# Optimization experiments

Hardware: AMD Instinct MI355X
Metric: run time of the kernel (lower is better)

## Reference

```python
import jax, jax.numpy as jnp
import numpy as np

B, S, D, H = 2, 2048, 2048, 16
HD = D // H  # 128


def setup_inputs() -> dict:
    key = jax.random.key(0)
    ks = jax.random.split(key, 6)
    sc = 0.02
    return {
        "x": jax.random.normal(ks[0], (B, S, D), jnp.float32),
        "attention_mask": jnp.ones((B, S), jnp.int32),
        "w_qkv": jax.random.normal(ks[1], (D, 3 * D), jnp.float32) * sc,
        "b_qkv": jnp.zeros((3 * D,), jnp.float32),
        "w_o": jax.random.normal(ks[2], (D, D), jnp.float32) * sc,
        "b_o": jnp.zeros((D,), jnp.float32),
        "ln1_w": jnp.ones((D,), jnp.float32),
        "w1": jax.random.normal(ks[3], (D, 8 * D), jnp.float32) * sc,
        "b1": jnp.zeros((8 * D,), jnp.float32),
        "w2": jax.random.normal(ks[4], (4 * D, D), jnp.float32) * sc,
        "b2": jnp.zeros((D,), jnp.float32),
        "ln2_w": jnp.ones((D,), jnp.float32),
    }


def rmsnorm(x, w, eps=1e-6):
    rms = jnp.sqrt(jnp.mean(x * x, axis=-1, keepdims=True) + eps)
    return w * (x / rms)


def rope_tables(seq_len, dim, base=10000.0):
    inv_freq = 1.0 / (base ** (jnp.arange(0, dim, 2, dtype=jnp.float32) / dim))
    t = jnp.arange(seq_len, dtype=jnp.float32)
    freqs = t[:, None] * inv_freq[None, :]          # [S, dim/2]
    emb = jnp.concatenate([freqs, freqs], axis=-1)  # [S, dim]
    return jnp.cos(emb), jnp.sin(emb)


def apply_rope(x, cos, sin):
    # Faithful to source: rotate pairs, then out = rot*cos + roll(rot,1)*sin
    xr = x.reshape(*x.shape[:-1], -1, 2)
    x1, x2 = xr[..., 0], xr[..., 1]
    rot = jnp.stack([-x2, x1], axis=-1).reshape(x.shape)
    return rot * cos + jnp.roll(rot, shift=1, axis=-1) * sin


def transformer_layer(x, attention_mask, w_qkv, b_qkv, w_o, b_o, ln1_w, w1, b1, w2, b2, ln2_w):
    residual = x
    qkv = x @ w_qkv + b_qkv                         # [B,S,3D]
    q, k, v = jnp.split(qkv, 3, axis=-1)
    split = lambda t: t.reshape(B, S, H, HD).transpose(0, 2, 1, 3)  # [B,H,S,HD]
    q, k, v = split(q), split(k), split(v)

    cos, sin = rope_tables(S, HD)                   # [S,HD], broadcasts over B,H
    q = apply_rope(q, cos, sin)
    k = apply_rope(k, cos, sin)

    scores = jnp.einsum("bhqd,bhkd->bhqk", q, k) / jnp.sqrt(jnp.float32(HD))
    mask = (attention_mask == 1)[:, None, None, :]  # [B,1,1,S]
    scores = jnp.where(mask, scores, -jnp.inf)
    attn = jax.nn.softmax(scores, axis=-1)
    out = jnp.einsum("bhqk,bhkd->bhqd", attn, v)
    out = out.transpose(0, 2, 1, 3).reshape(B, S, D)
    out = out @ w_o + b_o

    x = rmsnorm(out + residual, ln1_w)
    residual = x
    h = x @ w1 + b1                                 # [B,S,8D]
    h, gate = jnp.split(h, 2, axis=-1)
    h = h * jax.nn.gelu(gate, approximate=False)
    h = h @ w2 + b2
    return rmsnorm(h + residual, ln2_w)


def reference(x, attention_mask, w_qkv, b_qkv, w_o, b_o, ln1_w, w1, b1, w2, b2, ln2_w):
    return transformer_layer(x, attention_mask, w_qkv, b_qkv, w_o, b_o, ln1_w, w1, b1, w2, b2, ln2_w)
```

## Files before the change

### kernel.cpp

```cpp
#include <hip/hip_runtime.h>
#include <cstdint>

typedef unsigned short u16;
typedef __attribute__((ext_vector_type(8))) short short8;
typedef __attribute__((ext_vector_type(8))) unsigned short ushortx8;
typedef __attribute__((ext_vector_type(4))) float floatx4;

#define DEV __device__ __forceinline__

DEV u16 f2bf(float f) {
  union { float f; uint32_t u; } x; x.f = f;
  uint32_t r = x.u + 0x7fffu + ((x.u >> 16) & 1u);
  return (u16)(r >> 16);
}
DEV float bf2f(u16 h) {
  union { float f; uint32_t u; } x; x.u = ((uint32_t)h) << 16;
  return x.f;
}
DEV float fast_gelu(float g) {
  float u = 0.7978845608f * (g + 0.044715f * g * g * g);
  float e = __expf(-2.0f * fabsf(u));
  float th = (1.0f - e) / (1.0f + e);
  th = (u < 0.0f) ? -th : th;
  return 0.5f * g * (1.0f + th);
}
DEV void gload_lds16(const void* g, void* lds) {
  __builtin_amdgcn_global_load_lds(
      (const __attribute__((address_space(1))) char*)(uintptr_t)g,
      (__attribute__((address_space(3))) char*)(uintptr_t)lds, 16, 0, 0);
}


__global__ __launch_bounds__(256) void k_cvt_bf16(const float* __restrict__ in,
                                                  u16* __restrict__ out, int n) {
  int i = (blockIdx.x * 256 + threadIdx.x) * 8;
  if (i + 7 < n) {
    float4 a = *(const float4*)(in + i);
    float4 b = *(const float4*)(in + i + 4);
    ushortx8 o;
    o[0] = f2bf(a.x); o[1] = f2bf(a.y); o[2] = f2bf(a.z); o[3] = f2bf(a.w);
    o[4] = f2bf(b.x); o[5] = f2bf(b.y); o[6] = f2bf(b.z); o[7] = f2bf(b.w);
    *(ushortx8*)(out + i) = o;
  }
}

__global__ __launch_bounds__(256) void k_transpose_all(const float* __restrict__ Wq,
                                                       u16* __restrict__ WqT,
                                                       const float* __restrict__ Wo,
                                                       u16* __restrict__ WoT,
                                                       const float* __restrict__ W2,
                                                       u16* __restrict__ W2T) {
  __shared__ u16 t[64][70];
  int id = blockIdx.x;
  const float* W; u16* Wt; int R, C, tix;
  if (id < 3072)      { W = Wq; Wt = WqT; R = 2048; C = 6144; tix = id; }
  else if (id < 4096) { W = Wo; Wt = WoT; R = 2048; C = 2048; tix = id - 3072; }
  else                { W = W2; Wt = W2T; R = 8192; C = 2048; tix = id - 4096; }
  int ntc = C >> 6;
  int c0 = (tix % ntc) * 64, r0 = (tix / ntc) * 64;
  int cx = threadIdx.x & 15, ry = threadIdx.x >> 4;
#pragma unroll
  for (int i = 0; i < 4; ++i) {
    int row = ry + i * 16;
    float4 v = *(const float4*)(W + (size_t)(r0 + row) * C + c0 + cx * 4);
    ushort2 lo, hi;
    lo.x = f2bf(v.x); lo.y = f2bf(v.y);
    hi.x = f2bf(v.z); hi.y = f2bf(v.w);
    *(ushort2*)&t[row][cx * 4] = lo;
    *(ushort2*)&t[row][cx * 4 + 2] = hi;
  }
  __syncthreads();
#pragma unroll
  for (int i = 0; i < 4; ++i) {
    int col = ry + i * 16;
    ushort4 o;
    o.x = t[cx * 4 + 0][col]; o.y = t[cx * 4 + 1][col];
    o.z = t[cx * 4 + 2][col]; o.w = t[cx * 4 + 3][col];
    *(ushort4*)(Wt + (size_t)(c0 + col) * R + r0 + cx * 4) = o;
  }
}

__global__ __launch_bounds__(256) void k_transpose_w1p(const float* __restrict__ W,
                                                       u16* __restrict__ Wt) {
  __shared__ u16 t[64][70];
  int c0 = blockIdx.x * 64;
  int r0 = blockIdx.y * 64;
  int cx = threadIdx.x & 15, ry = threadIdx.x >> 4;
  int eta = c0 + cx * 4;
  int Bq = eta >> 8, ii = eta & 255, wn = (ii >> 6) & 3, rr = ii & 63, n = rr >> 4, tt = rr & 15;
  int src = Bq * 128 + wn * 32 + (n & 1) * 16 + tt + ((n >= 2) ? 8192 : 0);
#pragma unroll
  for (int i = 0; i < 4; ++i) {
    int row = ry + i * 16;
    float4 v = *(const float4*)(W + (size_t)(r0 + row) * 16384 + src);
    ushort2 lo, hi;
    lo.x = f2bf(v.x); lo.y = f2bf(v.y);
    hi.x = f2bf(v.z); hi.y = f2bf(v.w);
    *(ushort2*)&t[row][cx * 4] = lo;
    *(ushort2*)&t[row][cx * 4 + 2] = hi;
  }
  __syncthreads();
#pragma unroll
  for (int i = 0; i < 4; ++i) {
    int col = ry + i * 16;
    ushort4 o;
    o.x = t[cx * 4 + 0][col]; o.y = t[cx * 4 + 1][col];
    o.z = t[cx * 4 + 2][col]; o.w = t[cx * 4 + 3][col];
    *(ushort4*)(Wt + (size_t)(c0 + col + 0) * 0 +
                (size_t)(c0 + ry + i * 16) * 2048 + r0 + cx * 4) = o;
  }
}

__global__ __launch_bounds__(256) void k_rope_tab(float* __restrict__ ct, float* __restrict__ st) {
  int i = blockIdx.x * 256 + threadIdx.x;
  int s = i >> 6, j = i & 63;
  float invf = 1.0f / powf(10000.0f, (float)j * (1.0f / 64.0f));
  float ang = (float)s * invf;
  ct[i] = cosf(ang);
  st[i] = sinf(ang);
}

template <int EPI>
__global__ __launch_bounds__(512, 2) void k_gemm256(const u16* __restrict__ A,
                                                    const u16* __restrict__ Bt,
                                                    void* __restrict__ C,
                                                    const float* __restrict__ bias,
                                                    int M, int N, int K, int nsplit,
                                                    u16* __restrict__ qrO,
                                                    u16* __restrict__ krO,
                                                    u16* __restrict__ vtO,
                                                    const float* __restrict__ ctabO,
                                                    const float* __restrict__ stabO) {
  __shared__ __align__(16) u16 lds[4][2][8192];
  const int tid = threadIdx.x;
  const int w = tid >> 6, lane = tid & 63;
  const int l15 = lane & 15, l4 = lane >> 4;
  const int wm = w >> 2, wn = w & 3;
  const int nbn = N >> 8;
  const int nbm = M >> 8;

  int bm, bn, split = 0;
  if (nsplit == 1 && nbm == 16 && (nbn & 7) == 0) {
    const int xcd = blockIdx.x & 7, l = blockIdx.x >> 3;
    const int xr = xcd >> 1, xc = xcd & 1;
    const int stn = l >> 4, lbm = (l >> 2) & 3, lbn = l & 3;
    bm = xr * 4 + lbm;
    bn = xc * (nbn >> 1) + stn * 4 + lbn;
  } else {
    const int nwg = gridDim.x;
    const int q = nwg >> 3, r8 = nwg & 7;
    const int xcd = blockIdx.x & 7, loc = blockIdx.x >> 3;
    const int swz = (xcd < r8 ? xcd * (q + 1) : r8 * (q + 1) + (xcd - r8) * q) + loc;
    const int ntiles = nwg / nsplit;
    split = swz / ntiles;
    const int tix = swz % ntiles;
    bm = tix / nbn; bn = tix % nbn;
  }
  const int klen = K / nsplit;
  const int kofs = split * klen;

  const size_t abase = (size_t)bm * 256 * K + kofs;
  const size_t bbase = (size_t)bn * 256 * K + kofs;
  const int nt = klen >> 5;

  const int sr = tid >> 2;
  const int sc = (tid & 3) ^ ((sr >> 1) & 3);
  auto stage = [&](int kt, int li, int op) {
    const u16* src = op ? (Bt + bbase) : (A + abase);
    gload_lds16(src + (size_t)(li * 128 + sr) * K + kt * 32 + sc * 8,
                (void*)&lds[kt & 3][op][(li * 512 + w * 64) * 8]);
  };

  const int fro = l15 * 32 + (l4 ^ ((l15 >> 1) & 3)) * 8;

  floatx4 acc[8][4];
  floatx4 zero = {0.f, 0.f, 0.f, 0.f};
#pragma unroll
  for (int m = 0; m < 8; ++m)
#pragma unroll
    for (int n = 0; n < 4; ++n) acc[m][n] = zero;

  for (int kt = 0; kt < 3; ++kt)
    if (kt < nt) {
      stage(kt, 0, 0); stage(kt, 0, 1);
      stage(kt, 1, 0); stage(kt, 1, 1);
    }

  for (int t = 0; t < nt; ++t) {
    const int buf = t & 3;
    if (t < nt - 2)       asm volatile("s_waitcnt vmcnt(8)" ::: "memory");
    else if (t == nt - 2) asm volatile("s_waitcnt vmcnt(4)" ::: "memory");
    else                  asm volatile("s_waitcnt vmcnt(0)" ::: "memory");
    __builtin_amdgcn_sched_barrier(0);
    __builtin_amdgcn_s_barrier();
    const u16* Ab = &lds[buf][0][wm * 4096 + fro];
    const u16* Bb = &lds[buf][1][wn * 2048 + fro];
    short8 av[4], bv[4];
#pragma unroll
    for (int n = 0; n < 4; ++n) bv[n] = *(const short8*)(Bb + n * 512);
#pragma unroll
    for (int i = 0; i < 4; ++i) av[i] = *(const short8*)(Ab + i * 512);
    if (t + 3 < nt) { stage(t + 3, 0, 0); stage(t + 3, 0, 1); }
    asm volatile("s_waitcnt lgkmcnt(0)" ::: "memory");
    __builtin_amdgcn_sched_barrier(0);
    __builtin_amdgcn_s_setprio(1);
#pragma unroll
    for (int i = 0; i < 4; ++i)
#pragma unroll
      for (int n = 0; n < 4; ++n)
        acc[i][n] = __builtin_amdgcn_mfma_f32_16x16x32_bf16(av[i], bv[n], acc[i][n], 0, 0, 0);
    __builtin_amdgcn_s_setprio(0);
    __builtin_amdgcn_s_barrier();
#pragma unroll
    for (int i = 0; i < 4; ++i) av[i] = *(const short8*)(Ab + (4 + i) * 512);
    if (t + 3 < nt) { stage(t + 3, 1, 0); stage(t + 3, 1, 1); }
    asm volatile("s_waitcnt lgkmcnt(0)" ::: "memory");
    __builtin_amdgcn_sched_barrier(0);
    __builtin_amdgcn_s_setprio(1);
#pragma unroll
    for (int i = 0; i < 4; ++i)
#pragma unroll
      for (int n = 0; n < 4; ++n)
        acc[4 + i][n] = __builtin_amdgcn_mfma_f32_16x16x32_bf16(av[i], bv[n], acc[4 + i][n], 0, 0, 0);
    __builtin_amdgcn_s_setprio(0);
  }

  const int row0 = bm * 256 + wm * 128, col0 = bn * 256 + wn * 64;
  if (EPI == 2) {
    float* P = (float*)C + (size_t)split * M * N;
#pragma unroll
    for (int n = 0; n < 4; ++n) {
      int col = col0 + n * 16 + l15;
#pragma unroll
      for (int m = 0; m < 8; ++m)
#pragma unroll
        for (int j = 0; j < 4; ++j) {
          int row = row0 + m * 16 + l4 * 4 + j;
          P[(size_t)row * N + col] = acc[m][n][j];
        }
    }
  } else if (EPI == 3) {
    __syncthreads();
    u16* ep = ((u16*)lds) + w * 4096;
    const int colA = bn * 128 + wn * 32;
#pragma unroll
    for (int n = 0; n < 2; ++n) {
      float ba = bias[colA + n * 16 + l15];
      float bg = bias[8192 + colA + n * 16 + l15];
#pragma unroll
      for (int m = 0; m < 8; ++m)
#pragma unroll
        for (int j = 0; j < 4; ++j) {
          float a = acc[m][n][j] + ba;
          float g = acc[m][n + 2][j] + bg;
          ep[(m * 16 + l4 * 4 + j) * 32 + n * 16 + l15] = f2bf(a * fast_gelu(g));
        }
    }
    const int rr = lane >> 2, cg = lane & 3;
    u16* Cg = (u16*)C;
    const int Nact = N >> 1;
#pragma unroll
    for (int pass = 0; pass < 8; ++pass) {
      short8 v = *(const short8*)&ep[(pass * 16 + rr) * 32 + cg * 8];
      size_t grow = row0 + pass * 16 + rr;
      *(short8*)&Cg[grow * Nact + colA + cg * 8] = v;
    }
  } else if (EPI == 4) {
    constexpr int PAD = 264;
    u16* T = (u16*)lds;
    const int bq = bm >> 3;
    const int srow0 = (bm & 7) * 256;
#pragma unroll 1
    for (int hf = 0; hf < 2; ++hf) {
      __syncthreads();
      if (wm == hf) {
#pragma unroll
        for (int n = 0; n < 4; ++n) {
          float bb = bias[bn * 256 + wn * 64 + n * 16 + l15];
#pragma unroll
          for (int m = 0; m < 8; ++m)
#pragma unroll
            for (int j = 0; j < 4; ++j)
              T[(m * 16 + l4 * 4 + j) * PAD + wn * 64 + n * 16 + l15] =
                  f2bf(acc[m][n][j] + bb);
        }
      }
      __syncthreads();
      if (bn < 16) {
        int sl = tid >> 2, hh = (tid >> 1) & 1, t2 = tid & 1;
        const u16* row = T + sl * PAD + hh * 128;
        int s = srow0 + hf * 128 + sl;
        int head = 2 * (bn & 7) + hh;
        u16* dst = (bn < 8 ? qrO : krO) +
                   (((size_t)bq * 16 + head) * 2048 + s) * 128 + t2 * 64;
        const float* ctr = ctabO + (s << 6);
        const float* str2 = stabO + (s << 6);
#pragma unroll
        for (int ch = 0; ch < 8; ++ch) {
          int d0 = t2 * 64 + ch * 8;
          ushortx8 xv = *(const ushortx8*)(row + d0);
          float xp = bf2f(row[(d0 + 126) & 127]);
          int f0 = d0 & 63;
          float4 c0v = *(const float4*)(ctr + f0);
          float4 c1v = *(const float4*)(ctr + f0 + 4);
          float4 s0v = *(const float4*)(str2 + f0);
          float4 s1v = *(const float4*)(str2 + f0 + 4);
          float cc[8] = {c0v.x, c0v.y, c0v.z, c0v.w, c1v.x, c1v.y, c1v.z, c1v.w};
          float sn[8] = {s0v.x, s0v.y, s0v.z, s0v.w, s1v.x, s1v.y, s1v.z, s1v.w};
          ushortx8 o;
#pragma unroll
          for (int pr = 0; pr < 4; ++pr) {
            float xe = bf2f((u16)xv[2 * pr]), xo = bf2f((u16)xv[2 * pr + 1]);
            o[2 * pr]     = f2bf(-xo * cc[2 * pr] + xp * sn[2 * pr]);
            o[2 * pr + 1] = f2bf( xe * cc[2 * pr + 1] - xo * sn[2 * pr + 1]);
            xp = xe;
          }
          *(ushortx8*)(dst + ch * 8) = o;
        }
      } else {
        int hh = tid >> 8, dg = (tid >> 4) & 15, sc2 = tid & 15;
        int head = 2 * (bn - 16) + hh;
        int s0 = srow0 + hf * 128 + sc2 * 8;
        ushortx8 r[8];
#pragma unroll
        for (int i = 0; i < 8; ++i)
          r[i] = *(const ushortx8*)(T + (sc2 * 8 + i) * PAD + hh * 128 + dg * 8);
        u16* vbase = vtO + ((size_t)bq * 2048 + head * 128 + dg * 8) * 2048 + s0;
#pragma unroll
        for (int j2 = 0; j2 < 8; ++j2) {
          ushortx8 o;
#pragma unroll
          for (int i = 0; i < 8; ++i) o[i] = r[i][j2];
          *(ushortx8*)(vbase + (size_t)j2 * 2048) = o;
        }
      }
    }
  } else {
    __syncthreads();
    u16* ep = ((u16*)lds) + w * 8192;
#pragma unroll
    for (int n = 0; n < 4; ++n) {
      float bb = bias[col0 + n * 16 + l15];
#pragma unroll
      for (int m = 0; m < 8; ++m)
#pragma unroll
        for (int j = 0; j < 4; ++j)
          ep[(m * 16 + l4 * 4 + j) * 64 + n * 16 + l15] = f2bf(acc[m][n][j] + bb);
    }
    const int rr = lane >> 3, cg = lane & 7;
    u16* Cg = (u16*)C;
#pragma unroll
    for (int pass = 0; pass < 16; ++pass) {
      short8 v = *(const short8*)&ep[(pass * 8 + rr) * 64 + cg * 8];
      size_t grow = row0 + pass * 8 + rr;
      *(short8*)&Cg[grow * N + col0 + cg * 8] = v;
    }
  }
}

__global__ __launch_bounds__(512, 4) void k_attn(const u16* __restrict__ Qr,
                                                 const u16* __restrict__ Kr,
                                                 const u16* __restrict__ Vt,
                                                 const int* __restrict__ mask,
                                                 u16* __restrict__ O) {
  constexpr int S = 2048, HD = 128, H = 16;
  __shared__ __align__(16) u16 Ksh[64 * 128];
  __shared__ __align__(16) u16 Vsh[128 * 64];
  __shared__ __align__(16) u16 Psh[8][16 * 72];
  __shared__ float Msh[2048];

  const int bid = blockIdx.x;
  const int xcd = bid & 7, local = bid >> 3;
  const int bh = xcd * 4 + (local >> 4);
  const int qt = local & 15;
  const int b = bh >> 4, h = bh & 15;
  const int tid = threadIdx.x, wave = tid >> 6, lane = tid & 63;
  const int l15 = lane & 15, l4 = lane >> 4;
  const size_t bhs = (size_t)(b * H + h);
  const u16* Qb = Qr + bhs * S * HD;
  const u16* Kb = Kr + bhs * S * HD;
  const u16* Vb = Vt + bhs * HD * S;

  for (int i = tid; i < 2048; i += 512)
    Msh[i] = (mask[b * S + i] == 1) ? 0.0f : -1e30f;

  const int qrow = qt * 128 + wave * 16 + l15;
  short8 qf[4];
#pragma unroll
  for (int kk = 0; kk < 4; ++kk)
    qf[kk] = *(const short8*)&Qb[(size_t)qrow * HD + kk * 32 + l4 * 8];

  float m_run[4], l_run[4];
  floatx4 o_acc[8];
  floatx4 zero = {0.f, 0.f, 0.f, 0.f};
#pragma unroll
  for (int j = 0; j < 4; ++j) { m_run[j] = -1e30f; l_run[j] = 0.f; }
#pragma unroll
  for (int n = 0; n < 8; ++n) o_acc[n] = zero;

  for (int ktile = 0; ktile < S / 64; ++ktile) {
    __syncthreads();
#pragma unroll
    for (int it = 0; it < 2; ++it) {
      int gi = it * 512 + tid;
      {
        int row = gi >> 4, g = gi & 15;
        int gs = (g & 8) | ((g ^ row) & 7);
        gload_lds16(Kb + (size_t)(ktile * 64 + row) * HD + gs * 8,
                    (char*)&Ksh[it * 4096 + wave * 512]);
      }
      {
        int row = gi >> 3, g = gi & 7;
        int gs = (g ^ row) & 7;
        gload_lds16(Vb + (size_t)row * S + ktile * 64 + gs * 8,
                    (char*)&Vsh[it * 4096 + wave * 512]);
      }
    }
    __syncthreads();

    floatx4 s_acc[4];
#pragma unroll
    for (int nf = 0; nf < 4; ++nf) s_acc[nf] = zero;
    __builtin_amdgcn_s_setprio(1);
#pragma unroll
    for (int kk = 0; kk < 4; ++kk) {
#pragma unroll
      for (int nf = 0; nf < 4; ++nf) {
        int key = nf * 16 + l15;
        int G = kk * 4 + l4;
        int lg = (G & 8) | ((G ^ key) & 7);
        short8 kv = *(const short8*)&Ksh[key * 128 + lg * 8];
        s_acc[nf] = __builtin_amdgcn_mfma_f32_16x16x32_bf16(qf[kk], kv, s_acc[nf], 0, 0, 0);
      }
    }
    __builtin_amdgcn_s_setprio(0);

    const float scale = 0.08838834764831845f;
    float p[4][4];
#pragma unroll
    for (int nf = 0; nf < 4; ++nf) {
      float ma = Msh[ktile * 64 + nf * 16 + l15];
#pragma unroll
      for (int j = 0; j < 4; ++j) p[nf][j] = s_acc[nf][j] * scale + ma;
    }
#pragma unroll
    for (int j = 0; j < 4; ++j) {
      float mx = fmaxf(fmaxf(p[0][j], p[1][j]), fmaxf(p[2][j], p[3][j]));
      mx = fmaxf(mx, __shfl_xor(mx, 1));
      mx = fmaxf(mx, __shfl_xor(mx, 2));
      mx = fmaxf(mx, __shfl_xor(mx, 4));
      mx = fmaxf(mx, __shfl_xor(mx, 8));
      float mnew = fmaxf(m_run[j], mx);
      float corr = __expf(m_run[j] - mnew);
      float ps = 0.f;
#pragma unroll
      for (int nf = 0; nf < 4; ++nf) {
        p[nf][j] = __expf(p[nf][j] - mnew);
        ps += p[nf][j];
      }
      l_run[j] = l_run[j] * corr + ps;
      m_run[j] = mnew;
#pragma unroll
      for (int n = 0; n < 8; ++n) o_acc[n][j] *= corr;
    }

#pragma unroll
    for (int nf = 0; nf < 4; ++nf)
#pragma unroll
      for (int j = 0; j < 4; ++j)
        Psh[wave][(l4 * 4 + j) * 72 + nf * 16 + l15] = f2bf(p[nf][j]);

    __builtin_amdgcn_s_setprio(1);
#pragma unroll
    for (int ks = 0; ks < 2; ++ks) {
      short8 pa = *(const short8*)&Psh[wave][l15 * 72 + ks * 32 + l4 * 8];
#pragma unroll
      for (int nf2 = 0; nf2 < 8; ++nf2) {
        int hd = nf2 * 16 + l15;
        int G = ks * 4 + l4;
        short8 vv = *(const short8*)&Vsh[hd * 64 + ((G ^ hd) & 7) * 8];
        o_acc[nf2] = __builtin_amdgcn_mfma_f32_16x16x32_bf16(pa, vv, o_acc[nf2], 0, 0, 0);
      }
    }
    __builtin_amdgcn_s_setprio(0);
  }

#pragma unroll
  for (int j = 0; j < 4; ++j) {
    float ls = l_run[j];
    ls += __shfl_xor(ls, 1); ls += __shfl_xor(ls, 2);
    ls += __shfl_xor(ls, 4); ls += __shfl_xor(ls, 8);
    l_run[j] = ls;
  }

#pragma unroll
  for (int j = 0; j < 4; ++j) {
    float inv = 1.0f / l_run[j];
    int srow = qt * 128 + wave * 16 + l4 * 4 + j;
    size_t orow = ((size_t)b * S + srow) * 2048 + h * 128;
#pragma unroll
    for (int nf2 = 0; nf2 < 8; ++nf2)
      O[orow + nf2 * 16 + l15] = f2bf(o_acc[nf2][j] * inv);
  }
}

__global__ __launch_bounds__(256) void k_rms_fuse1(const float* __restrict__ p0,
                                                   const float* __restrict__ p1,
                                                   const float* __restrict__ bias,
                                                   const float* __restrict__ resid,
                                                   const float* __restrict__ w,
                                                   u16* __restrict__ ob) {
  int row = blockIdx.x;
  int t = threadIdx.x;
  size_t base = (size_t)row * 2048 + t * 8;
  float4 a0 = *(const float4*)(p0 + base);
  float4 a1 = *(const float4*)(p0 + base + 4);
  float4 b0 = *(const float4*)(p1 + base);
  float4 b1 = *(const float4*)(p1 + base + 4);
  float4 r0 = *(const float4*)(resid + base);
  float4 r1 = *(const float4*)(resid + base + 4);
  float4 c0 = *(const float4*)(bias + t * 8);
  float4 c1 = *(const float4*)(bias + t * 8 + 4);
  float v[8];
  v[0] = a0.x + b0.x + r0.x + c0.x; v[1] = a0.y + b0.y + r0.y + c0.y;
  v[2] = a0.z + b0.z + r0.z + c0.z; v[3] = a0.w + b0.w + r0.w + c0.w;
  v[4] = a1.x + b1.x + r1.x + c1.x; v[5] = a1.y + b1.y + r1.y + c1.y;
  v[6] = a1.z + b1.z + r1.z + c1.z; v[7] = a1.w + b1.w + r1.w + c1.w;
  float ss = 0.f;
#pragma unroll
  for (int e = 0; e < 8; ++e) ss += v[e] * v[e];
#pragma unroll
  for (int d = 1; d < 64; d <<= 1) ss += __shfl_xor(ss, d);
  __shared__ float sred[4];
  if ((t & 63) == 0) sred[t >> 6] = ss;
  __syncthreads();
  float tot = sred[0] + sred[1] + sred[2] + sred[3];
  float scale = rsqrtf(tot * (1.0f / 2048.0f) + 1e-6f);
  const float* wp = w + t * 8;
  ushort4 q0, q1;
  q0.x = f2bf(v[0] * wp[0] * scale); q0.y = f2bf(v[1] * wp[1] * scale);
  q0.z = f2bf(v[2] * wp[2] * scale); q0.w = f2bf(v[3] * wp[3] * scale);
  q1.x = f2bf(v[4] * wp[4] * scale); q1.y = f2bf(v[5] * wp[5] * scale);
  q1.z = f2bf(v[6] * wp[6] * scale); q1.w = f2bf(v[7] * wp[7] * scale);
  *(ushort4*)(ob + base) = q0;
  *(ushort4*)(ob + base + 4) = q1;
}

__global__ __launch_bounds__(256) void k_rms_fuse2(const float* __restrict__ p0,
                                                   const float* __restrict__ p1,
                                                   const float* __restrict__ bias,
                                                   const u16* __restrict__ residb,
                                                   const float* __restrict__ w,
                                                   float* __restrict__ of) {
  int row = blockIdx.x;
  int t = threadIdx.x;
  size_t base = (size_t)row * 2048 + t * 8;
  float4 a0 = *(const float4*)(p0 + base);
  float4 a1 = *(const float4*)(p0 + base + 4);
  float4 b0 = *(const float4*)(p1 + base);
  float4 b1 = *(const float4*)(p1 + base + 4);
  ushortx8 rb = *(const ushortx8*)(residb + base);
  float4 c0 = *(const float4*)(bias + t * 8);
  float4 c1 = *(const float4*)(bias + t * 8 + 4);
  float v[8];
  v[0] = a0.x + b0.x + c0.x; v[1] = a0.y + b0.y + c0.y;
  v[2] = a0.z + b0.z + c0.z; v[3] = a0.w + b0.w + c0.w;
  v[4] = a1.x + b1.x + c1.x; v[5] = a1.y + b1.y + c1.y;
  v[6] = a1.z + b1.z + c1.z; v[7] = a1.w + b1.w + c1.w;
#pragma unroll
  for (int e = 0; e < 8; ++e) v[e] += bf2f((u16)rb[e]);
  float ss = 0.f;
#pragma unroll
  for (int e = 0; e < 8; ++e) ss += v[e] * v[e];
#pragma unroll
  for (int d = 1; d < 64; d <<= 1) ss += __shfl_xor(ss, d);
  __shared__ float sred[4];
  if ((t & 63) == 0) sred[t >> 6] = ss;
  __syncthreads();
  float tot = sred[0] + sred[1] + sred[2] + sred[3];
  float scale = rsqrtf(tot * (1.0f / 2048.0f) + 1e-6f);
  const float* wp = w + t * 8;
  float4 f0, f1;
  f0.x = v[0] * wp[0] * scale; f0.y = v[1] * wp[1] * scale;
  f0.z = v[2] * wp[2] * scale; f0.w = v[3] * wp[3] * scale;
  f1.x = v[4] * wp[4] * scale; f1.y = v[5] * wp[5] * scale;
  f1.z = v[6] * wp[6] * scale; f1.w = v[7] * wp[7] * scale;
  *(float4*)(of + base) = f0;
  *(float4*)(of + base + 4) = f1;
}

extern "C" void kernel_launch(void* const* d_in, const int* in_sizes, int n_in,
                              void* d_out, int out_size, void* d_ws, size_t ws_size,
                              hipStream_t stream) {
  const float* x     = (const float*)d_in[0];
  const int*   amask = (const int*)d_in[1];
  const float* w_qkv = (const float*)d_in[2];
  const float* b_qkv = (const float*)d_in[3];
  const float* w_o   = (const float*)d_in[4];
  const float* b_o   = (const float*)d_in[5];
  const float* ln1_w = (const float*)d_in[6];
  const float* w1    = (const float*)d_in[7];
  const float* b1    = (const float*)d_in[8];
  const float* w2    = (const float*)d_in[9];
  const float* b2    = (const float*)d_in[10];
  const float* ln2_w = (const float*)d_in[11];
  float* out = (float*)d_out;

  char* ws = (char*)d_ws;
  u16*   xb    = (u16*)(ws + 0);
  u16*   wqkvT = (u16*)(ws + 16777216);
  u16*   woT   = (u16*)(ws + 41943040);
  u16*   w1Tp  = (u16*)(ws + 50331648);
  u16*   w2T   = (u16*)(ws + 117440512);
  float* ctab  = (float*)(ws + 150994944);
  float* stab  = (float*)(ws + 151519232);
  u16*   qr    = (u16*)(ws + 202375168);
  u16*   kr    = (u16*)(ws + 219152384);
  u16*   vt    = (u16*)(ws + 235929600);
  u16*   aout  = (u16*)(ws + 252706816);
  u16*   x1b   = (u16*)(ws + 303038464);
  float* p01a  = (float*)(ws + 152043520);
  u16*   act   = (u16*)(ws + 152043520);
  float* p01b  = (float*)(ws + 219152384);

  k_cvt_bf16<<<4096, 256, 0, stream>>>(x, xb, 4096 * 2048);
  k_transpose_all<<<8192, 256, 0, stream>>>(w_qkv, wqkvT, w_o, woT, w2, w2T);
  k_transpose_w1p<<<dim3(256, 32), 256, 0, stream>>>(w1, w1Tp);
  k_rope_tab<<<512, 256, 0, stream>>>(ctab, stab);

  k_gemm256<4><<<16 * 24, 512, 0, stream>>>(xb, wqkvT, nullptr, b_qkv,
                                            4096, 6144, 2048, 1,
                                            qr, kr, vt, ctab, stab);
  k_attn<<<512, 512, 0, stream>>>(qr, kr, vt, amask, aout);

  k_gemm256<2><<<16 * 8 * 2, 512, 0, stream>>>(aout, woT, p01a, nullptr,
                                               4096, 2048, 2048, 2,
                                               nullptr, nullptr, nullptr, nullptr, nullptr);
  k_rms_fuse1<<<4096, 256, 0, stream>>>(p01a, p01a + (size_t)4096 * 2048, b_o, x, ln1_w, x1b);

  k_gemm256<3><<<16 * 64, 512, 0, stream>>>(x1b, w1Tp, act, b1,
                                            4096, 16384, 2048, 1,
                                            nullptr, nullptr, nullptr, nullptr, nullptr);

  k_gemm256<2><<<16 * 8 * 2, 512, 0, stream>>>(act, w2T, p01b, nullptr,
                                               4096, 2048, 8192, 2,
                                               nullptr, nullptr, nullptr, nullptr, nullptr);
  k_rms_fuse2<<<4096, 256, 0, stream>>>(p01b, p01b + (size_t)4096 * 2048, b2, x1b, ln2_w, out);
}
```

Before: 829.7 us.

## Prefetch next K/V tile into registers during attention compute

Replaces the synchronous global-to-LDS direct loads in the flash-attention loop with register prefetching. The next tile's K/V loads are issued after the current tile is written to LDS, so global latency overlaps with the MFMA work. The load addresses are precomputed once outside the loop. This costs extra VGPRs, which may lower occupancy, and relies on manual waitcnt and barriers. It also tidies a weight-transpose store expression without changing its result.

```diff
diff --git a/kernel.cpp b/kernel.cpp
--- a/kernel.cpp
+++ b/kernel.cpp
@@ -102,12 +102,11 @@
   __syncthreads();
 #pragma unroll
   for (int i = 0; i < 4; ++i) {
+    ushort4 o;
     int col = ry + i * 16;
-    ushort4 o;
     o.x = t[cx * 4 + 0][col]; o.y = t[cx * 4 + 1][col];
     o.z = t[cx * 4 + 2][col]; o.w = t[cx * 4 + 3][col];
-    *(ushort4*)(Wt + (size_t)(c0 + col + 0) * 0 +
-                (size_t)(c0 + ry + i * 16) * 2048 + r0 + cx * 4) = o;
+    *(ushort4*)(Wt + (size_t)(c0 + col) * 2048 + r0 + cx * 4) = o;
   }
 }
 
@@ -390,6 +389,20 @@
   for (int kk = 0; kk < 4; ++kk)
     qf[kk] = *(const short8*)&Qb[(size_t)qrow * HD + kk * 32 + l4 * 8];
 
+  const int giA = tid, giB = 512 + tid;
+  const int rKA = giA >> 4, gKA = giA & 15;
+  const int rKB = giB >> 4, gKB = giB & 15;
+  const int gsKA = (gKA & 8) | ((gKA ^ rKA) & 7);
+  const int gsKB = (gKB & 8) | ((gKB ^ rKB) & 7);
+  const int rVA = giA >> 3, gVA = giA & 7;
+  const int rVB = giB >> 3, gVB = giB & 7;
+  const int gsVA = (gVA ^ rVA) & 7;
+  const int gsVB = (gVB ^ rVB) & 7;
+  const u16* pKA = Kb + (size_t)rKA * HD + gsKA * 8;
+  const u16* pKB = Kb + (size_t)rKB * HD + gsKB * 8;
+  const u16* pVA = Vb + (size_t)rVA * S + gsVA * 8;
+  const u16* pVB = Vb + (size_t)rVB * S + gsVB * 8;
+
   float m_run[4], l_run[4];
   floatx4 o_acc[8];
   floatx4 zero = {0.f, 0.f, 0.f, 0.f};
@@ -398,25 +411,29 @@
 #pragma unroll
   for (int n = 0; n < 8; ++n) o_acc[n] = zero;
 
+  uint4 k0 = *(const uint4*)pKA;
+  uint4 k1 = *(const uint4*)pKB;
+  uint4 v0 = *(const uint4*)pVA;
+  uint4 v1 = *(const uint4*)pVB;
+
   for (int ktile = 0; ktile < S / 64; ++ktile) {
-    __syncthreads();
-#pragma unroll
-    for (int it = 0; it < 2; ++it) {
-      int gi = it * 512 + tid;
-      {
-        int row = gi >> 4, g = gi & 15;
-        int gs = (g & 8) | ((g ^ row) & 7);
-        gload_lds16(Kb + (size_t)(ktile * 64 + row) * HD + gs * 8,
-                    (char*)&Ksh[it * 4096 + wave * 512]);
-      }
-      {
-        int row = gi >> 3, g = gi & 7;
-        int gs = (g ^ row) & 7;
-        gload_lds16(Vb + (size_t)row * S + ktile * 64 + gs * 8,
-                    (char*)&Vsh[it * 4096 + wave * 512]);
-      }
-    }
-    __syncthreads();
+    __builtin_amdgcn_sched_barrier(0);
+    __builtin_amdgcn_s_barrier();
+    __builtin_amdgcn_sched_barrier(0);
+    *(uint4*)&Ksh[(size_t)(0 * 512 + tid) * 8] = k0;
+    *(uint4*)&Ksh[(size_t)(1 * 512 + tid) * 8] = k1;
+    *(uint4*)&Vsh[(size_t)(0 * 512 + tid) * 8] = v0;
+    *(uint4*)&Vsh[(size_t)(1 * 512 + tid) * 8] = v1;
+    if (ktile + 1 < S / 64) {
+      k0 = *(const uint4*)(pKA + (size_t)(ktile + 1) * 8192);
+      k1 = *(const uint4*)(pKB + (size_t)(ktile + 1) * 8192);
+      v0 = *(const uint4*)(pVA + (size_t)(ktile + 1) * 64);
+      v1 = *(const uint4*)(pVB + (size_t)(ktile + 1) * 64);
+    }
+    asm volatile("s_waitcnt lgkmcnt(0)" ::: "memory");
+    __builtin_amdgcn_sched_barrier(0);
+    __builtin_amdgcn_s_barrier();
+    __builtin_amdgcn_sched_barrier(0);
 
     floatx4 s_acc[4];
 #pragma unroll
```

New measurement: 832.1 us. About the same (+0.3%).
